# Performance work log

Measured on AMD Instinct MI355X. Metric: run time of the kernel, lower is better.

## Reference

```python
import jax, jax.numpy as jnp
import numpy as np
from jax import lax

B, T, D = 4, 1024, 512      # batch, seq_len, d_model
L = 4                        # n_layers
N = 16                       # d_state
DC = 4                       # d_conv
DI = 2 * D                   # d_inner = expand * d_model
DTR = D // 16                # dt_rank
H = 128                      # head hidden dim
EPS = 1e-5


def layer_norm(x, g, b):
    mu = jnp.mean(x, axis=-1, keepdims=True)
    var = jnp.mean((x - mu) ** 2, axis=-1, keepdims=True)
    return (x - mu) * lax.rsqrt(var + EPS) * g + b


def setup_inputs() -> dict:
    key = jax.random.key(0)
    ks = jax.random.split(key, 24)
    s = 0.02
    return {
        "daily_summaries": jax.random.normal(ks[0], (B, T, D), jnp.float32),
        # per-layer mamba params, stacked on leading L axis
        "in_proj_w": s * jax.random.normal(ks[1], (L, 2 * DI, D), jnp.float32),
        "conv_w": s * jax.random.normal(ks[2], (L, DI, DC), jnp.float32),
        "conv_b": jnp.zeros((L, DI), jnp.float32),
        "x_proj_w": s * jax.random.normal(ks[3], (L, DTR + 2 * N, DI), jnp.float32),
        "dt_proj_w": s * jax.random.normal(ks[4], (L, DI, DTR), jnp.float32),
        "dt_proj_b": jnp.full((L, DI), -4.0, jnp.float32),  # softplus -> small dt
        "A_log": jnp.log(jnp.broadcast_to(jnp.arange(1, N + 1, dtype=jnp.float32), (L, DI, N))),
        "D_skip": jnp.ones((L, DI), jnp.float32),
        "out_proj_w": s * jax.random.normal(ks[5], (L, D, DI), jnp.float32),
        "ln_g": jnp.ones((L, D), jnp.float32),
        "ln_b": jnp.zeros((L, D), jnp.float32),
        # attention pooling
        "attn_w": s * jax.random.normal(ks[6], (1, D), jnp.float32),
        "attn_b": jnp.zeros((1,), jnp.float32),
        # VIX head
        "h1_w": s * jax.random.normal(ks[7], (H, D), jnp.float32),
        "h1_b": jnp.zeros((H,), jnp.float32),
        "ln1_g": jnp.ones((H,), jnp.float32),
        "ln1_b": jnp.zeros((H,), jnp.float32),
        "h2_w": s * jax.random.normal(ks[8], (H, H), jnp.float32),
        "h2_b": jnp.zeros((H,), jnp.float32),
        "ln2_g": jnp.ones((H,), jnp.float32),
        "ln2_b": jnp.zeros((H,), jnp.float32),
        # note: torch zero-inits the final layer; we use random so grads are nonzero
        "h3_w": s * jax.random.normal(ks[9], (1, H), jnp.float32),
        "h3_b": jnp.zeros((1,), jnp.float32),
    }


def mamba_layer(x, in_w, cw, cb, xp_w, dt_w, dt_b, A_log, D_skip, out_w):
    """x: [B,T,D] -> [B,T,D]; canonical Mamba selective scan."""
    xz = jnp.einsum('btd,ed->bte', x, in_w)          # [B,T,2*DI]
    x_in, z = jnp.split(xz, 2, axis=-1)
    # causal depthwise conv over time
    xc = lax.conv_general_dilated(
        x_in.transpose(0, 2, 1), cw[:, None, :], (1,), [(DC - 1, 0)],
        feature_group_count=DI, dimension_numbers=('NCH', 'OIH', 'NCH'))
    xc = jax.nn.silu(xc + cb[None, :, None]).transpose(0, 2, 1)   # [B,T,DI]
    dbc = jnp.einsum('btd,ed->bte', xc, xp_w)        # [B,T,DTR+2N]
    dt_r, Bm, Cm = dbc[..., :DTR], dbc[..., DTR:DTR + N], dbc[..., DTR + N:]
    dt = jax.nn.softplus(jnp.einsum('btr,dr->btd', dt_r, dt_w) + dt_b)  # [B,T,DI]
    A = -jnp.exp(A_log)                              # [DI,N]
    dA = jnp.exp(dt[..., None] * A)                  # [B,T,DI,N]
    dBx = dt[..., None] * Bm[:, :, None, :] * xc[..., None]  # [B,T,DI,N]

    def step(h, inp):
        dA_t, dBx_t, C_t = inp
        h = dA_t * h + dBx_t                         # [B,DI,N]
        return h, jnp.einsum('bdn,bn->bd', h, C_t)

    h0 = jnp.zeros((x.shape[0], DI, N), x.dtype)
    _, ys = lax.scan(step, h0, (dA.transpose(1, 0, 2, 3),
                                dBx.transpose(1, 0, 2, 3),
                                Cm.transpose(1, 0, 2)))
    y = ys.transpose(1, 0, 2) + xc * D_skip          # [B,T,DI]
    y = y * jax.nn.silu(z)
    return jnp.einsum('btd,ed->bte', y, out_w)       # [B,T,D]


def reference(daily_summaries, in_proj_w, conv_w, conv_b, x_proj_w, dt_proj_w,
              dt_proj_b, A_log, D_skip, out_proj_w, ln_g, ln_b, attn_w, attn_b,
              h1_w, h1_b, ln1_g, ln1_b, h2_w, h2_b, ln2_g, ln2_b, h3_w, h3_b):
    x = daily_summaries  # proj is Identity (d_model_l1 == d_model)
    for l in range(L):
        residual = x
        y = mamba_layer(x, in_proj_w[l], conv_w[l], conv_b[l], x_proj_w[l],
                        dt_proj_w[l], dt_proj_b[l], A_log[l], D_skip[l], out_proj_w[l])
        x = layer_norm(y, ln_g[l], ln_b[l]) + residual
    # attention pooling (no mask)
    scores = jnp.einsum('btd,od->bto', x, attn_w) + attn_b   # [B,T,1]
    w = jax.nn.softmax(scores, axis=1)
    pooled = jnp.sum(w * x, axis=1)                          # [B,D]
    # VIX head: Linear -> LN -> GELU (x2) -> Linear
    h1 = jax.nn.gelu(layer_norm(pooled @ h1_w.T + h1_b, ln1_g, ln1_b), approximate=False)
    h2 = jax.nn.gelu(layer_norm(h1 @ h2_w.T + h2_b, ln2_g, ln2_b), approximate=False)
    return (h2 @ h3_w.T + h3_b).squeeze(-1)                  # [B]
```

## Files before the change

kernel.cpp:

```cpp
#include <hip/hip_runtime.h>
#include <hip/hip_bf16.h>
#include <math.h>

#define BATCH 4
#define TLEN 1024
#define DMODEL 512
#define DINNER 1024
#define NSTATE 16
#define EPSV 1e-5f
#define NC 32
#define CT 32
#define DSTR 36
#define LOG2E 1.44269504088896f

typedef __attribute__((ext_vector_type(8))) short bf16x8;
typedef __attribute__((ext_vector_type(4))) float f32x4;

__device__ inline unsigned short f2bf(float f) {
  union { float f; unsigned int u; } c; c.f = f;
  unsigned int u = c.u;
  return (unsigned short)((u + 0x7FFFu + ((u >> 16) & 1u)) >> 16);
}
__device__ inline float bf2f(unsigned short u) {
  union { unsigned int i; float f; } c;
  c.i = ((unsigned int)u) << 16;
  return c.f;
}

__device__ inline float warpReduceSum(float v) {
#pragma unroll
  for (int o = 32; o > 0; o >>= 1) v += __shfl_down(v, o, 64);
  return v;
}
__device__ inline float warpReduceMax(float v) {
#pragma unroll
  for (int o = 32; o > 0; o >>= 1) v = fmaxf(v, __shfl_down(v, o, 64));
  return v;
}
__device__ inline float2 blockReduceSum2_256(float a, float b) {
  __shared__ float sma[4], smb[4];
  int lane = threadIdx.x & 63, wid = threadIdx.x >> 6;
#pragma unroll
  for (int o = 32; o > 0; o >>= 1) { a += __shfl_down(a, o, 64); b += __shfl_down(b, o, 64); }
  if (lane == 0) { sma[wid] = a; smb[wid] = b; }
  __syncthreads();
  float ra = sma[0] + sma[1] + sma[2] + sma[3];
  float rb = smb[0] + smb[1] + smb[2] + smb[3];
  __syncthreads();
  return make_float2(ra, rb);
}
__device__ inline float blockReduceSum256(float v) {
  __shared__ float sm[4];
  int lane = threadIdx.x & 63, wid = threadIdx.x >> 6;
  v = warpReduceSum(v);
  if (lane == 0) sm[wid] = v;
  __syncthreads();
  float r = sm[0] + sm[1] + sm[2] + sm[3];
  __syncthreads();
  return r;
}
__device__ inline float blockReduceMax256(float v) {
  __shared__ float sm[4];
  int lane = threadIdx.x & 63, wid = threadIdx.x >> 6;
  v = warpReduceMax(v);
  if (lane == 0) sm[wid] = v;
  __syncthreads();
  float r = fmaxf(fmaxf(sm[0], sm[1]), fmaxf(sm[2], sm[3]));
  __syncthreads();
  return r;
}
__device__ inline float blockReduceSum128(float v) {
  __shared__ float sm[2];
  int lane = threadIdx.x & 63, wid = threadIdx.x >> 6;
  v = warpReduceSum(v);
  if (lane == 0) sm[wid] = v;
  __syncthreads();
  float r = sm[0] + sm[1];
  __syncthreads();
  return r;
}

__global__ void __launch_bounds__(256)
cast_f32_bf16(const float* __restrict__ src, unsigned short* __restrict__ dst, int n) {
  int i = (blockIdx.x * 256 + threadIdx.x) * 4;
  if (i >= n) return;
  float4 v = *(const float4*)(src + i);
  dst[i + 0] = f2bf(v.x);
  dst[i + 1] = f2bf(v.y);
  dst[i + 2] = f2bf(v.z);
  dst[i + 3] = f2bf(v.w);
}

#define LDP 72
__global__ void __launch_bounds__(256)
gemm_bf16_split(const unsigned short* __restrict__ A, int lda,
                const unsigned short* __restrict__ B, int ldb,
                unsigned short* __restrict__ Cx, unsigned short* __restrict__ Cz, int K) {
  __shared__ unsigned short As[128 * LDP];
  __shared__ unsigned short Bs[128 * LDP];
  const int tid = threadIdx.x;
  const int lane = tid & 63, wid = tid >> 6;
  const int wm = wid >> 1, wn = wid & 1;
  const int row0 = blockIdx.y * 128, col0 = blockIdx.x * 128;
  const int c8 = (tid & 7) * 8;
  const int r0 = tid >> 3;
  const int l15 = lane & 15, lq = lane >> 4;
  f32x4 acc[4][4] = {};
  for (int k0 = 0; k0 < K; k0 += 64) {
#pragma unroll
    for (int p = 0; p < 4; p++) {
      int row = r0 + p * 32;
      bf16x8 av = *(const bf16x8*)(A + (size_t)(row0 + row) * lda + k0 + c8);
      bf16x8 bv = *(const bf16x8*)(B + (size_t)(col0 + row) * ldb + k0 + c8);
      *(bf16x8*)(As + row * LDP + c8) = av;
      *(bf16x8*)(Bs + row * LDP + c8) = bv;
    }
    __syncthreads();
#pragma unroll
    for (int s = 0; s < 2; s++) {
      const int koff = s * 32 + lq * 8;
      bf16x8 af[4], bfr[4];
#pragma unroll
      for (int i = 0; i < 4; i++)
        af[i] = *(const bf16x8*)(As + (wm * 64 + i * 16 + l15) * LDP + koff);
#pragma unroll
      for (int j = 0; j < 4; j++)
        bfr[j] = *(const bf16x8*)(Bs + (wn * 64 + j * 16 + l15) * LDP + koff);
#pragma unroll
      for (int i = 0; i < 4; i++)
#pragma unroll
        for (int j = 0; j < 4; j++)
          acc[i][j] = __builtin_amdgcn_mfma_f32_16x16x32_bf16(af[i], bfr[j], acc[i][j], 0, 0, 0);
    }
    __syncthreads();
  }
  unsigned short* dst = (col0 < 1024) ? Cx : Cz;
  const int cb = (col0 < 1024) ? col0 : (col0 - 1024);
#pragma unroll
  for (int i = 0; i < 4; i++)
#pragma unroll
    for (int j = 0; j < 4; j++)
#pragma unroll
      for (int r = 0; r < 4; r++) {
        int row = row0 + wm * 64 + i * 16 + lq * 4 + r;
        int col = cb + wn * 64 + j * 16 + l15;
        dst[(size_t)row * 1024 + col] = f2bf(acc[i][j][r]);
      }
}

__global__ void __launch_bounds__(256)
gemm_bf16_n64(const unsigned short* __restrict__ A, int lda,
              const unsigned short* __restrict__ B, int ldb,
              float* __restrict__ C, int ldc, int K) {
  __shared__ unsigned short As[128 * LDP];
  __shared__ unsigned short Bs[64 * LDP];
  const int tid = threadIdx.x;
  const int lane = tid & 63, wid = tid >> 6;
  const int wm = wid >> 1, wn = wid & 1;
  const int row0 = blockIdx.y * 128, col0 = blockIdx.x * 64;
  const int c8 = (tid & 7) * 8;
  const int r0 = tid >> 3;
  const int l15 = lane & 15, lq = lane >> 4;
  f32x4 acc[4][2] = {};
  for (int k0 = 0; k0 < K; k0 += 64) {
#pragma unroll
    for (int p = 0; p < 4; p++) {
      int row = r0 + p * 32;
      bf16x8 av = *(const bf16x8*)(A + (size_t)(row0 + row) * lda + k0 + c8);
      *(bf16x8*)(As + row * LDP + c8) = av;
    }
#pragma unroll
    for (int p = 0; p < 2; p++) {
      int row = r0 + p * 32;
      bf16x8 bv = *(const bf16x8*)(B + (size_t)(col0 + row) * ldb + k0 + c8);
      *(bf16x8*)(Bs + row * LDP + c8) = bv;
    }
    __syncthreads();
#pragma unroll
    for (int s = 0; s < 2; s++) {
      const int koff = s * 32 + lq * 8;
      bf16x8 af[4], bfr[2];
#pragma unroll
      for (int i = 0; i < 4; i++)
        af[i] = *(const bf16x8*)(As + (wm * 64 + i * 16 + l15) * LDP + koff);
#pragma unroll
      for (int j = 0; j < 2; j++)
        bfr[j] = *(const bf16x8*)(Bs + (wn * 32 + j * 16 + l15) * LDP + koff);
#pragma unroll
      for (int i = 0; i < 4; i++)
#pragma unroll
        for (int j = 0; j < 2; j++)
          acc[i][j] = __builtin_amdgcn_mfma_f32_16x16x32_bf16(af[i], bfr[j], acc[i][j], 0, 0, 0);
    }
    __syncthreads();
  }
#pragma unroll
  for (int i = 0; i < 4; i++)
#pragma unroll
    for (int j = 0; j < 2; j++)
#pragma unroll
      for (int r = 0; r < 4; r++) {
        int row = row0 + wm * 64 + i * 16 + lq * 4 + r;
        int col = col0 + wn * 32 + j * 16 + l15;
        C[(size_t)row * ldc + col] = acc[i][j][r];
      }
}

__global__ void __launch_bounds__(256)
gemm_bf16_n64_sk(const unsigned short* __restrict__ A, int lda,
                 const unsigned short* __restrict__ B, int ldb,
                 float* __restrict__ Cpart, int KCH) {
  __shared__ unsigned short As[128 * LDP];
  __shared__ unsigned short Bs[64 * LDP];
  const int tid = threadIdx.x;
  const int lane = tid & 63, wid = tid >> 6;
  const int wm = wid >> 1, wn = wid & 1;
  const int row0 = blockIdx.y * 128, col0 = 0;
  const int kbase = blockIdx.z * KCH;
  float* Cz = Cpart + (size_t)blockIdx.z * 4096 * 64;
  const int c8 = (tid & 7) * 8;
  const int r0 = tid >> 3;
  const int l15 = lane & 15, lq = lane >> 4;
  f32x4 acc[4][2] = {};
  for (int k0 = 0; k0 < KCH; k0 += 64) {
#pragma unroll
    for (int p = 0; p < 4; p++) {
      int row = r0 + p * 32;
      bf16x8 av = *(const bf16x8*)(A + (size_t)(row0 + row) * lda + kbase + k0 + c8);
      *(bf16x8*)(As + row * LDP + c8) = av;
    }
#pragma unroll
    for (int p = 0; p < 2; p++) {
      int row = r0 + p * 32;
      bf16x8 bv = *(const bf16x8*)(B + (size_t)(col0 + row) * ldb + kbase + k0 + c8);
      *(bf16x8*)(Bs + row * LDP + c8) = bv;
    }
    __syncthreads();
#pragma unroll
    for (int s = 0; s < 2; s++) {
      const int koff = s * 32 + lq * 8;
      bf16x8 af[4], bfr[2];
#pragma unroll
      for (int i = 0; i < 4; i++)
        af[i] = *(const bf16x8*)(As + (wm * 64 + i * 16 + l15) * LDP + koff);
#pragma unroll
      for (int j = 0; j < 2; j++)
        bfr[j] = *(const bf16x8*)(Bs + (wn * 32 + j * 16 + l15) * LDP + koff);
#pragma unroll
      for (int i = 0; i < 4; i++)
#pragma unroll
        for (int j = 0; j < 2; j++)
          acc[i][j] = __builtin_amdgcn_mfma_f32_16x16x32_bf16(af[i], bfr[j], acc[i][j], 0, 0, 0);
    }
    __syncthreads();
  }
#pragma unroll
  for (int i = 0; i < 4; i++)
#pragma unroll
    for (int j = 0; j < 2; j++)
#pragma unroll
      for (int r = 0; r < 4; r++) {
        int row = row0 + wm * 64 + i * 16 + lq * 4 + r;
        int col = wn * 32 + j * 16 + l15;
        Cz[(size_t)row * 64 + col] = acc[i][j][r];
      }
}

__global__ void __launch_bounds__(256)
reduce4_kernel(const float* __restrict__ part, float* __restrict__ out, int n) {
  int i = (blockIdx.x * 256 + threadIdx.x) * 4;
  if (i >= n) return;
  float4 a = *(const float4*)(part + i);
  float4 b = *(const float4*)(part + n + i);
  float4 c = *(const float4*)(part + 2 * n + i);
  float4 d = *(const float4*)(part + 3 * n + i);
  float4 r;
  r.x = a.x + b.x + c.x + d.x;
  r.y = a.y + b.y + c.y + d.y;
  r.z = a.z + b.z + c.z + d.z;
  r.w = a.w + b.w + c.w + d.w;
  *(float4*)(out + i) = r;
}

__global__ void __launch_bounds__(256)
gemm_dt(const float* __restrict__ A, const float* __restrict__ B,
        unsigned short* __restrict__ C, const float* __restrict__ bias) {
  __shared__ __align__(16) float As[16][68];
  __shared__ __align__(16) float Bs[16][68];
  const int tid = threadIdx.x;
  const int tx = tid & 15, ty = tid >> 4;
  const int row0 = blockIdx.y * 64, col0 = blockIdx.x * 64;
  float acc[4][4] = {};
  for (int k0 = 0; k0 < 32; k0 += 16) {
#pragma unroll
    for (int i = 0; i < 4; i++) {
      int e = tid + i * 256;
      int m = e >> 4, kk = e & 15;
      As[kk][m] = A[(size_t)(row0 + m) * 64 + k0 + kk];
      Bs[kk][m] = B[(size_t)(col0 + m) * 32 + k0 + kk];
    }
    __syncthreads();
#pragma unroll
    for (int kk = 0; kk < 16; kk++) {
      float4 a4 = *(const float4*)&As[kk][ty << 2];
      float4 b4 = *(const float4*)&Bs[kk][tx << 2];
      float a[4] = {a4.x, a4.y, a4.z, a4.w};
      float b[4] = {b4.x, b4.y, b4.z, b4.w};
#pragma unroll
      for (int i = 0; i < 4; i++)
#pragma unroll
        for (int j = 0; j < 4; j++) acc[i][j] = fmaf(a[i], b[j], acc[i][j]);
    }
    __syncthreads();
  }
#pragma unroll
  for (int i = 0; i < 4; i++) {
    size_t r = row0 + (ty << 2) + i;
#pragma unroll
    for (int j = 0; j < 4; j++) {
      int c = col0 + (tx << 2) + j;
      float v = acc[i][j] + bias[c];
      v = (v > 20.f) ? v : log1pf(__expf(v));
      C[r * 1024 + c] = f2bf(v);
    }
  }
}

__global__ void conv_silu_kernel(const unsigned short* __restrict__ xinbf,
                                 const float* __restrict__ cw,
                                 const float* __restrict__ cb,
                                 unsigned short* __restrict__ xcbf) {
  int idx = blockIdx.x * 256 + threadIdx.x;
  int d = idx & 1023;
  int bt = idx >> 10;
  int t = bt & 1023;
  float acc = cb[d];
  const float* w = cw + d * 4;
#pragma unroll
  for (int k = 0; k < 4; k++) {
    int ts = t - 3 + k;
    if (ts >= 0) acc = fmaf(bf2f(xinbf[((size_t)bt + (ts - t)) * 1024 + d]), w[k], acc);
  }
  float sig = 1.f / (1.f + __expf(-acc));
  xcbf[idx] = f2bf(acc * sig);
}

__global__ void __launch_bounds__(256)
scan_part1(const unsigned short* __restrict__ dtbf, const unsigned short* __restrict__ xcbf,
           const float* __restrict__ dbc, const float* __restrict__ A_log,
           float* __restrict__ hloc, float* __restrict__ sdtb) {
  __shared__ unsigned short dts[64 * DSTR];
  __shared__ unsigned short xcs[64 * DSTR];
  __shared__ float Bsh[CT * 20];
  const int chunk = blockIdx.x, dg = blockIdx.y, b = blockIdx.z;
  const int tid = threadIdx.x;
  const int ch = tid >> 2, q4 = (tid & 3) * 4;
  const int d = dg * 64 + ch;
  const size_t bt0 = (size_t)b * TLEN + chunk * CT;
  for (int i = tid; i < CT * 64; i += 256) {
    int t = i >> 6, c = i & 63;
    size_t bt = bt0 + t;
    dts[c * DSTR + t] = dtbf[bt * 1024 + dg * 64 + c];
    xcs[c * DSTR + t] = xcbf[bt * 1024 + dg * 64 + c];
  }
  for (int i = tid; i < CT * 16; i += 256) {
    int t = i >> 4, n = i & 15;
    Bsh[t * 20 + n] = dbc[(bt0 + t) * 64 + 32 + n];
  }
  __syncthreads();
  float4 al = *(const float4*)&A_log[d * 16 + q4];
  float4 A;
  A.x = -__expf(al.x) * LOG2E; A.y = -__expf(al.y) * LOG2E;
  A.z = -__expf(al.z) * LOG2E; A.w = -__expf(al.w) * LOG2E;
  float4 h = {0.f, 0.f, 0.f, 0.f};
  float sdt = 0.f;
#pragma unroll
  for (int t0 = 0; t0 < CT; t0 += 4) {
    ushort4 d4 = *(const ushort4*)&dts[ch * DSTR + t0];
    ushort4 x4 = *(const ushort4*)&xcs[ch * DSTR + t0];
    const float dta[4] = {bf2f(d4.x), bf2f(d4.y), bf2f(d4.z), bf2f(d4.w)};
    const float xca[4] = {bf2f(x4.x), bf2f(x4.y), bf2f(x4.z), bf2f(x4.w)};
#pragma unroll
    for (int u = 0; u < 4; u++) {
      float dtv = dta[u];
      float4 B4 = *(const float4*)&Bsh[(t0 + u) * 20 + q4];
      float uin = dtv * xca[u];
      h.x = fmaf(exp2f(dtv * A.x), h.x, uin * B4.x);
      h.y = fmaf(exp2f(dtv * A.y), h.y, uin * B4.y);
      h.z = fmaf(exp2f(dtv * A.z), h.z, uin * B4.z);
      h.w = fmaf(exp2f(dtv * A.w), h.w, uin * B4.w);
      sdt += dtv;
    }
  }
  size_t slab = (size_t)(b * 16 + dg);
  *(float4*)&hloc[(slab * NC + chunk) * 1024 + tid * 4] = h;
  sdtb[(slab * NC + chunk) * 256 + tid] = sdt;
}

__global__ void __launch_bounds__(256)
scan_prefix(const float* __restrict__ A_log, const float* __restrict__ hloc,
            const float* __restrict__ sdtb, float* __restrict__ h0buf) {
  const int slab = blockIdx.x;
  const int tid = threadIdx.x;
  const int dg = slab & 15;
  const int ch = tid >> 2, q4 = (tid & 3) * 4;
  const int d = dg * 64 + ch;
  float4 al = *(const float4*)&A_log[d * 16 + q4];
  float4 A;
  A.x = -__expf(al.x) * LOG2E; A.y = -__expf(al.y) * LOG2E;
  A.z = -__expf(al.z) * LOG2E; A.w = -__expf(al.w) * LOG2E;
  float4 h = {0.f, 0.f, 0.f, 0.f};
  size_t base = (size_t)slab * NC;
  for (int c = 0; c < NC; c++) {
    *(float4*)&h0buf[(base + c) * 1024 + tid * 4] = h;
    float4 hl = *(const float4*)&hloc[(base + c) * 1024 + tid * 4];
    float s = sdtb[(base + c) * 256 + tid];
    h.x = fmaf(exp2f(s * A.x), h.x, hl.x);
    h.y = fmaf(exp2f(s * A.y), h.y, hl.y);
    h.z = fmaf(exp2f(s * A.z), h.z, hl.z);
    h.w = fmaf(exp2f(s * A.w), h.w, hl.w);
  }
}

__global__ void __launch_bounds__(256)
scan_part2(const unsigned short* __restrict__ dtbf, const unsigned short* __restrict__ xcbf,
           const float* __restrict__ dbc, const unsigned short* __restrict__ zbf,
           const float* __restrict__ A_log, const float* __restrict__ Dsk,
           const float* __restrict__ h0buf, unsigned short* __restrict__ ybf) {
  __shared__ unsigned short dts[64 * DSTR];
  __shared__ unsigned short xcs[64 * DSTR];
  __shared__ float Bsh[CT * 20];
  __shared__ float Csh[CT * 20];
  __shared__ float ys[CT * 64];
  const int chunk = blockIdx.x, dg = blockIdx.y, b = blockIdx.z;
  const int tid = threadIdx.x;
  const int q = tid & 3;
  const int ch = tid >> 2, q4 = q * 4;
  const int d = dg * 64 + ch;
  const size_t bt0 = (size_t)b * TLEN + chunk * CT;
  const size_t slab = (size_t)(b * 16 + dg);
  float4 h = *(const float4*)&h0buf[(slab * NC + chunk) * 1024 + tid * 4];
  float4 al = *(const float4*)&A_log[d * 16 + q4];
  float4 A;
  A.x = -__expf(al.x) * LOG2E; A.y = -__expf(al.y) * LOG2E;
  A.z = -__expf(al.z) * LOG2E; A.w = -__expf(al.w) * LOG2E;
  for (int i = tid; i < CT * 64; i += 256) {
    int t = i >> 6, c = i & 63;
    size_t bt = bt0 + t;
    dts[c * DSTR + t] = dtbf[bt * 1024 + dg * 64 + c];
    xcs[c * DSTR + t] = xcbf[bt * 1024 + dg * 64 + c];
  }
  for (int i = tid; i < CT * 16; i += 256) {
    int t = i >> 4, n = i & 15;
    Bsh[t * 20 + n] = dbc[(bt0 + t) * 64 + 32 + n];
    Csh[t * 20 + n] = dbc[(bt0 + t) * 64 + 48 + n];
  }
  __syncthreads();
  const float Dv = Dsk[d];
#pragma unroll
  for (int t0 = 0; t0 < CT; t0 += 4) {
    ushort4 d4 = *(const ushort4*)&dts[ch * DSTR + t0];
    ushort4 x4 = *(const ushort4*)&xcs[ch * DSTR + t0];
    const float dta[4] = {bf2f(d4.x), bf2f(d4.y), bf2f(d4.z), bf2f(d4.w)};
    const float xca[4] = {bf2f(x4.x), bf2f(x4.y), bf2f(x4.z), bf2f(x4.w)};
#pragma unroll
    for (int u = 0; u < 4; u++) {
      float dtv = dta[u];
      float4 B4 = *(const float4*)&Bsh[(t0 + u) * 20 + q4];
      float4 C4 = *(const float4*)&Csh[(t0 + u) * 20 + q4];
      float uin = dtv * xca[u];
      h.x = fmaf(exp2f(dtv * A.x), h.x, uin * B4.x);
      h.y = fmaf(exp2f(dtv * A.y), h.y, uin * B4.y);
      h.z = fmaf(exp2f(dtv * A.z), h.z, uin * B4.z);
      h.w = fmaf(exp2f(dtv * A.w), h.w, uin * B4.w);
      float cs = h.x * C4.x + h.y * C4.y + h.z * C4.z + h.w * C4.w;
      cs += __shfl_xor(cs, 1, 4);
      cs += __shfl_xor(cs, 2, 4);
      if (q == 0) ys[(t0 + u) * 64 + ch] = cs + xca[u] * Dv;
    }
  }
  __syncthreads();
  for (int i = tid; i < CT * 64; i += 256) {
    int t = i >> 6, c = i & 63;
    size_t bt = bt0 + t;
    float zv = bf2f(zbf[bt * 1024 + dg * 64 + c]);
    float sig = 1.f / (1.f + __expf(-zv));
    ybf[bt * 1024 + dg * 64 + c] = f2bf(ys[t * 64 + c] * (zv * sig));
  }
}

__global__ void __launch_bounds__(256)
ln_res_kernel(const float* __restrict__ mo, const float* __restrict__ res,
              const float* __restrict__ g, const float* __restrict__ bb,
              float* __restrict__ xout, unsigned short* __restrict__ xout_bf) {
  int row = blockIdx.x;
  int tid = threadIdx.x;
  size_t base = (size_t)row * 512;
  float v0 = mo[base + tid], v1 = mo[base + tid + 256];
  float2 ss = blockReduceSum2_256(v0 + v1, v0 * v0 + v1 * v1);
  float mu = ss.x * (1.f / 512.f);
  float var = ss.y * (1.f / 512.f) - mu * mu;
  float rs = rsqrtf(var + EPSV);
  float o0 = (v0 - mu) * rs * g[tid] + bb[tid] + res[base + tid];
  float o1 = (v1 - mu) * rs * g[tid + 256] + bb[tid + 256] + res[base + tid + 256];
  xout[base + tid] = o0;
  xout[base + tid + 256] = o1;
  xout_bf[base + tid] = f2bf(o0);
  xout_bf[base + tid + 256] = f2bf(o1);
}

__global__ void __launch_bounds__(256)
score_kernel(const unsigned short* __restrict__ x, const float* __restrict__ aw,
             const float* __restrict__ ab, float* __restrict__ sc) {
  int row = blockIdx.x * 4 + (threadIdx.x >> 6);
  int lane = threadIdx.x & 63;
  size_t base = (size_t)row * 512;
  float p = 0.f;
#pragma unroll
  for (int j = 0; j < 8; j++)
    p = fmaf(bf2f(x[base + lane + 64 * j]), aw[lane + 64 * j], p);
  p = warpReduceSum(p);
  if (lane == 0) sc[row] = p + ab[0];
}

__global__ void __launch_bounds__(256)
softmax_t_kernel(const float* __restrict__ sc, float* __restrict__ wsm) {
  int b = blockIdx.x, tid = threadIdx.x;
  float v[4];
  float m = -INFINITY;
#pragma unroll
  for (int j = 0; j < 4; j++) { v[j] = sc[b * 1024 + tid + 256 * j]; m = fmaxf(m, v[j]); }
  m = blockReduceMax256(m);
  float s = 0.f;
#pragma unroll
  for (int j = 0; j < 4; j++) { v[j] = __expf(v[j] - m); s += v[j]; }
  s = blockReduceSum256(s);
  float inv = 1.f / s;
#pragma unroll
  for (int j = 0; j < 4; j++) wsm[b * 1024 + tid + 256 * j] = v[j] * inv;
}

__global__ void __launch_bounds__(256)
pool_partial(const unsigned short* __restrict__ x, const float* __restrict__ wsm,
             float* __restrict__ partial) {
  int tc = blockIdx.x, b = blockIdx.y, tid = threadIdx.x;
  float a0 = 0.f, a1 = 0.f;
  for (int t = tc * 32; t < tc * 32 + 32; t++) {
    float wv = wsm[b * 1024 + t];
    size_t base = ((size_t)b * 1024 + t) * 512;
    a0 = fmaf(wv, bf2f(x[base + tid]), a0);
    a1 = fmaf(wv, bf2f(x[base + tid + 256]), a1);
  }
  size_t pb = ((size_t)b * 32 + tc) * 512;
  partial[pb + tid] = a0;
  partial[pb + tid + 256] = a1;
}

__global__ void __launch_bounds__(256)
pool_reduce(const float* __restrict__ partial, float* __restrict__ pooled) {
  int b = blockIdx.x, tid = threadIdx.x;
  float a0 = 0.f, a1 = 0.f;
  for (int tc = 0; tc < 32; tc++) {
    size_t pb = ((size_t)b * 32 + tc) * 512;
    a0 += partial[pb + tid];
    a1 += partial[pb + tid + 256];
  }
  pooled[b * 512 + tid] = a0;
  pooled[b * 512 + tid + 256] = a1;
}

__device__ inline float gelu_exact(float x) {
  return 0.5f * x * (1.f + erff(x * 0.70710678118654752f));
}
__global__ void __launch_bounds__(128)
head_kernel(const float* __restrict__ pooled,
            const float* __restrict__ h1w, const float* __restrict__ h1b,
            const float* __restrict__ g1, const float* __restrict__ b1,
            const float* __restrict__ h2w, const float* __restrict__ h2b,
            const float* __restrict__ g2, const float* __restrict__ b2,
            const float* __restrict__ h3w, const float* __restrict__ h3b,
            float* __restrict__ out) {
  int tid = threadIdx.x;
  int b = blockIdx.x;
  __shared__ float hs[128];
  float s = h1b[tid];
  const float* p = pooled + b * 512;
  for (int d = 0; d < 512; d += 4) {
    float4 pv = *(const float4*)(p + d);
    float4 wv = *(const float4*)(h1w + tid * 512 + d);
    s = fmaf(pv.x, wv.x, s); s = fmaf(pv.y, wv.y, s);
    s = fmaf(pv.z, wv.z, s); s = fmaf(pv.w, wv.w, s);
  }
  float mu = blockReduceSum128(s) * (1.f / 128.f);
  float dd = s - mu;
  float var = blockReduceSum128(dd * dd) * (1.f / 128.f);
  float v = dd * rsqrtf(var + EPSV) * g1[tid] + b1[tid];
  hs[tid] = gelu_exact(v);
  __syncthreads();
  float s2 = h2b[tid];
  for (int j = 0; j < 128; j++) s2 = fmaf(hs[j], h2w[tid * 128 + j], s2);
  float mu2 = blockReduceSum128(s2) * (1.f / 128.f);
  float d2 = s2 - mu2;
  float var2 = blockReduceSum128(d2 * d2) * (1.f / 128.f);
  float v2 = d2 * rsqrtf(var2 + EPSV) * g2[tid] + b2[tid];
  float h2v = gelu_exact(v2);
  float o = blockReduceSum128(h2v * h3w[tid]);
  if (tid == 0) out[b] = o + h3b[0];
}

extern "C" void kernel_launch(void* const* d_in, const int* in_sizes, int n_in,
                              void* d_out, int out_size, void* d_ws, size_t ws_size,
                              hipStream_t stream) {
  (void)in_sizes; (void)n_in; (void)out_size; (void)ws_size;
  const float* x0   = (const float*)d_in[0];
  const float* inw  = (const float*)d_in[1];
  const float* cw   = (const float*)d_in[2];
  const float* cb   = (const float*)d_in[3];
  const float* xpw  = (const float*)d_in[4];
  const float* dtw  = (const float*)d_in[5];
  const float* dtb  = (const float*)d_in[6];
  const float* alog = (const float*)d_in[7];
  const float* dsk  = (const float*)d_in[8];
  const float* outw = (const float*)d_in[9];
  const float* lng  = (const float*)d_in[10];
  const float* lnb  = (const float*)d_in[11];
  const float* aw   = (const float*)d_in[12];
  const float* ab   = (const float*)d_in[13];
  const float* h1w  = (const float*)d_in[14];
  const float* h1b  = (const float*)d_in[15];
  const float* g1   = (const float*)d_in[16];
  const float* b1   = (const float*)d_in[17];
  const float* h2w  = (const float*)d_in[18];
  const float* h2b  = (const float*)d_in[19];
  const float* g2   = (const float*)d_in[20];
  const float* b2   = (const float*)d_in[21];
  const float* h3w  = (const float*)d_in[22];
  const float* h3b  = (const float*)d_in[23];

  float* ws = (float*)d_ws;
  unsigned short* xinbf = (unsigned short*)ws;
  unsigned short* zbf   = xinbf + 4194304;
  unsigned short* xcbf  = zbf + 4194304;
  unsigned short* dtbf  = xcbf + 4194304;
  float* dbc     = (float*)(dtbf + 4194304);
  float* xpart   = dbc + 262144;
  float* mo      = xpart + 1048576;
  float* xbuf    = mo + 2097152;
  float* hloc    = xbuf + 2097152;
  float* sdtb    = hloc + 2097152;
  float* h0buf   = sdtb + 524288;
  float* scores  = h0buf + 2097152;
  float* wsm     = scores + 4096;
  float* partial = wsm + 4096;
  float* pooled  = partial + 65536;
  unsigned short* abuf    = (unsigned short*)(pooled + 2048);
  unsigned short* ybf     = abuf + 2097152;
  unsigned short* wbf_in  = ybf + 4194304;
  unsigned short* wbf_out = wbf_in + 4194304;
  unsigned short* wbf_xp  = wbf_out + 2097152;

  cast_f32_bf16<<<4096, 256, 0, stream>>>(inw, wbf_in, 4194304);
  cast_f32_bf16<<<2048, 256, 0, stream>>>(outw, wbf_out, 2097152);
  cast_f32_bf16<<<256, 256, 0, stream>>>(xpw, wbf_xp, 262144);
  cast_f32_bf16<<<2048, 256, 0, stream>>>(x0, abuf, 2097152);

  const float* xcur = x0;
  for (int l = 0; l < 4; l++) {
    gemm_bf16_split<<<dim3(16, 32), 256, 0, stream>>>(
        abuf, 512, wbf_in + (size_t)l * 2048 * 512, 512, xinbf, zbf, 512);
    conv_silu_kernel<<<16384, 256, 0, stream>>>(xinbf, cw + l * 4096, cb + l * 1024, xcbf);
    gemm_bf16_n64_sk<<<dim3(1, 32, 4), 256, 0, stream>>>(
        xcbf, 1024, wbf_xp + (size_t)l * 65536, 1024, xpart, 256);
    reduce4_kernel<<<256, 256, 0, stream>>>(xpart, dbc, 262144);
    gemm_dt<<<dim3(16, 64), 256, 0, stream>>>(
        dbc, dtw + (size_t)l * 32768, dtbf, dtb + l * 1024);
    scan_part1<<<dim3(NC, 16, 4), 256, 0, stream>>>(
        dtbf, xcbf, dbc, alog + (size_t)l * 16384, hloc, sdtb);
    scan_prefix<<<64, 256, 0, stream>>>(alog + (size_t)l * 16384, hloc, sdtb, h0buf);
    scan_part2<<<dim3(NC, 16, 4), 256, 0, stream>>>(
        dtbf, xcbf, dbc, zbf, alog + (size_t)l * 16384, dsk + l * 1024, h0buf, ybf);
    gemm_bf16_n64<<<dim3(8, 32), 256, 0, stream>>>(
        ybf, 1024, wbf_out + (size_t)l * 524288, 1024, mo, 512, 1024);
    ln_res_kernel<<<4096, 256, 0, stream>>>(mo, xcur, lng + l * 512, lnb + l * 512,
                                            xbuf, abuf);
    xcur = xbuf;
  }
  score_kernel<<<1024, 256, 0, stream>>>(abuf, aw, ab, scores);
  softmax_t_kernel<<<4, 256, 0, stream>>>(scores, wsm);
  pool_partial<<<dim3(32, 4), 256, 0, stream>>>(abuf, wsm, partial);
  pool_reduce<<<4, 256, 0, stream>>>(partial, pooled);
  head_kernel<<<4, 128, 0, stream>>>(pooled, h1w, h1b, g1, b1, h2w, h2b, g2, b2,
                                     h3w, h3b, (float*)d_out);
}
```

Before: 762.2 us.

## Fuse dt projection into scan kernels, vectorize conv, fold scores into layernorm

Removes the separate gemm_dt kernel and its bf16 dt buffer. Each scan kernel now computes dt = softplus(dbc[:, :32] @ dt_w^T + b) in shared memory from the dbc tile it already loads. The depthwise conv+SiLU kernel now processes four channels per thread with vector loads. The attention score dot product is folded into the final layer's layernorm kernel, which drops score_kernel. The trade-off is that the dt projection is computed twice, once in each scan pass, and shared memory use per block goes up.

Result: slower. 778.7 us (+2.2%).

```diff
diff --git a/kernel.cpp b/kernel.cpp
--- a/kernel.cpp
+++ b/kernel.cpp
@@ -215,7 +215,7 @@
   const int tid = threadIdx.x;
   const int lane = tid & 63, wid = tid >> 6;
   const int wm = wid >> 1, wn = wid & 1;
-  const int row0 = blockIdx.y * 128, col0 = 0;
+  const int row0 = blockIdx.y * 128;
   const int kbase = blockIdx.z * KCH;
   float* Cz = Cpart + (size_t)blockIdx.z * 4096 * 64;
   const int c8 = (tid & 7) * 8;
@@ -232,7 +232,7 @@
 #pragma unroll
     for (int p = 0; p < 2; p++) {
       int row = r0 + p * 32;
-      bf16x8 bv = *(const bf16x8*)(B + (size_t)(col0 + row) * ldb + kbase + k0 + c8);
+      bf16x8 bv = *(const bf16x8*)(B + (size_t)row * ldb + kbase + k0 + c8);
       *(bf16x8*)(Bs + row * LDP + c8) = bv;
     }
     __syncthreads();
@@ -283,75 +283,52 @@
 }
 
 __global__ void __launch_bounds__(256)
-gemm_dt(const float* __restrict__ A, const float* __restrict__ B,
-        unsigned short* __restrict__ C, const float* __restrict__ bias) {
-  __shared__ __align__(16) float As[16][68];
-  __shared__ __align__(16) float Bs[16][68];
-  const int tid = threadIdx.x;
-  const int tx = tid & 15, ty = tid >> 4;
-  const int row0 = blockIdx.y * 64, col0 = blockIdx.x * 64;
-  float acc[4][4] = {};
-  for (int k0 = 0; k0 < 32; k0 += 16) {
-#pragma unroll
-    for (int i = 0; i < 4; i++) {
-      int e = tid + i * 256;
-      int m = e >> 4, kk = e & 15;
-      As[kk][m] = A[(size_t)(row0 + m) * 64 + k0 + kk];
-      Bs[kk][m] = B[(size_t)(col0 + m) * 32 + k0 + kk];
-    }
-    __syncthreads();
-#pragma unroll
-    for (int kk = 0; kk < 16; kk++) {
-      float4 a4 = *(const float4*)&As[kk][ty << 2];
-      float4 b4 = *(const float4*)&Bs[kk][tx << 2];
-      float a[4] = {a4.x, a4.y, a4.z, a4.w};
-      float b[4] = {b4.x, b4.y, b4.z, b4.w};
-#pragma unroll
-      for (int i = 0; i < 4; i++)
-#pragma unroll
-        for (int j = 0; j < 4; j++) acc[i][j] = fmaf(a[i], b[j], acc[i][j]);
-    }
-    __syncthreads();
-  }
-#pragma unroll
-  for (int i = 0; i < 4; i++) {
-    size_t r = row0 + (ty << 2) + i;
-#pragma unroll
-    for (int j = 0; j < 4; j++) {
-      int c = col0 + (tx << 2) + j;
-      float v = acc[i][j] + bias[c];
-      v = (v > 20.f) ? v : log1pf(__expf(v));
-      C[r * 1024 + c] = f2bf(v);
-    }
-  }
-}
-
-__global__ void conv_silu_kernel(const unsigned short* __restrict__ xinbf,
-                                 const float* __restrict__ cw,
-                                 const float* __restrict__ cb,
-                                 unsigned short* __restrict__ xcbf) {
+conv_silu_kernel(const unsigned short* __restrict__ xinbf,
+                 const float* __restrict__ cw,
+                 const float* __restrict__ cb,
+                 unsigned short* __restrict__ xcbf) {
   int idx = blockIdx.x * 256 + threadIdx.x;
-  int d = idx & 1023;
-  int bt = idx >> 10;
+  int d4 = (idx & 255) * 4;
+  int bt = idx >> 8;
   int t = bt & 1023;
-  float acc = cb[d];
-  const float* w = cw + d * 4;
+  float4 bias4 = *(const float4*)(cb + d4);
+  float a0 = bias4.x, a1 = bias4.y, a2 = bias4.z, a3 = bias4.w;
+  float4 w0 = *(const float4*)(cw + (size_t)(d4 + 0) * 4);
+  float4 w1 = *(const float4*)(cw + (size_t)(d4 + 1) * 4);
+  float4 w2 = *(const float4*)(cw + (size_t)(d4 + 2) * 4);
+  float4 w3 = *(const float4*)(cw + (size_t)(d4 + 3) * 4);
+  const float k0[4] = {w0.x, w0.y, w0.z, w0.w};
+  const float k1[4] = {w1.x, w1.y, w1.z, w1.w};
+  const float k2[4] = {w2.x, w2.y, w2.z, w2.w};
+  const float k3[4] = {w3.x, w3.y, w3.z, w3.w};
 #pragma unroll
   for (int k = 0; k < 4; k++) {
     int ts = t - 3 + k;
-    if (ts >= 0) acc = fmaf(bf2f(xinbf[((size_t)bt + (ts - t)) * 1024 + d]), w[k], acc);
-  }
-  float sig = 1.f / (1.f + __expf(-acc));
-  xcbf[idx] = f2bf(acc * sig);
-}
-
-__global__ void __launch_bounds__(256)
-scan_part1(const unsigned short* __restrict__ dtbf, const unsigned short* __restrict__ xcbf,
-           const float* __restrict__ dbc, const float* __restrict__ A_log,
+    if (ts >= 0) {
+      ushort4 xv = *(const ushort4*)(xinbf + ((size_t)bt + (ts - t)) * 1024 + d4);
+      a0 = fmaf(bf2f(xv.x), k0[k], a0);
+      a1 = fmaf(bf2f(xv.y), k1[k], a1);
+      a2 = fmaf(bf2f(xv.z), k2[k], a2);
+      a3 = fmaf(bf2f(xv.w), k3[k], a3);
+    }
+  }
+  ushort4 outv;
+  outv.x = f2bf(a0 / (1.f + __expf(-a0)));
+  outv.y = f2bf(a1 / (1.f + __expf(-a1)));
+  outv.z = f2bf(a2 / (1.f + __expf(-a2)));
+  outv.w = f2bf(a3 / (1.f + __expf(-a3)));
+  *(ushort4*)(xcbf + (size_t)bt * 1024 + d4) = outv;
+}
+
+__global__ void __launch_bounds__(256)
+scan_part1(const unsigned short* __restrict__ xcbf,
+           const float* __restrict__ dbc, const float* __restrict__ dtw,
+           const float* __restrict__ dtbias, const float* __restrict__ A_log,
            float* __restrict__ hloc, float* __restrict__ sdtb) {
+  __shared__ float dbcs[CT * 68];
+  __shared__ float dtws[64 * 33];
   __shared__ unsigned short dts[64 * DSTR];
   __shared__ unsigned short xcs[64 * DSTR];
-  __shared__ float Bsh[CT * 20];
   const int chunk = blockIdx.x, dg = blockIdx.y, b = blockIdx.z;
   const int tid = threadIdx.x;
   const int ch = tid >> 2, q4 = (tid & 3) * 4;
@@ -359,13 +336,27 @@
   const size_t bt0 = (size_t)b * TLEN + chunk * CT;
   for (int i = tid; i < CT * 64; i += 256) {
     int t = i >> 6, c = i & 63;
-    size_t bt = bt0 + t;
-    dts[c * DSTR + t] = dtbf[bt * 1024 + dg * 64 + c];
-    xcs[c * DSTR + t] = xcbf[bt * 1024 + dg * 64 + c];
-  }
-  for (int i = tid; i < CT * 16; i += 256) {
-    int t = i >> 4, n = i & 15;
-    Bsh[t * 20 + n] = dbc[(bt0 + t) * 64 + 32 + n];
+    dbcs[t * 68 + c] = dbc[(bt0 + t) * 64 + c];
+    xcs[c * DSTR + t] = xcbf[(bt0 + t) * 1024 + dg * 64 + c];
+  }
+  for (int i = tid; i < 64 * 32; i += 256) {
+    int c = i >> 5, k = i & 31;
+    dtws[c * 33 + k] = dtw[(size_t)(dg * 64 + c) * 32 + k];
+  }
+  __syncthreads();
+  {
+    const int chd = tid & 63, tq = tid >> 6;
+    const float bias = dtbias[dg * 64 + chd];
+#pragma unroll
+    for (int jj = 0; jj < 8; jj++) {
+      int t = tq * 8 + jj;
+      float acc = bias;
+#pragma unroll
+      for (int k = 0; k < 32; k++)
+        acc = fmaf(dbcs[t * 68 + k], dtws[chd * 33 + k], acc);
+      acc = (acc > 20.f) ? acc : log1pf(__expf(acc));
+      dts[chd * DSTR + t] = f2bf(acc);
+    }
   }
   __syncthreads();
   float4 al = *(const float4*)&A_log[d * 16 + q4];
@@ -383,7 +374,7 @@
 #pragma unroll
     for (int u = 0; u < 4; u++) {
       float dtv = dta[u];
-      float4 B4 = *(const float4*)&Bsh[(t0 + u) * 20 + q4];
+      float4 B4 = *(const float4*)&dbcs[(t0 + u) * 68 + 32 + q4];
       float uin = dtv * xca[u];
       h.x = fmaf(exp2f(dtv * A.x), h.x, uin * B4.x);
       h.y = fmaf(exp2f(dtv * A.y), h.y, uin * B4.y);
@@ -423,15 +414,15 @@
 }
 
 __global__ void __launch_bounds__(256)
-scan_part2(const unsigned short* __restrict__ dtbf, const unsigned short* __restrict__ xcbf,
-           const float* __restrict__ dbc, const unsigned short* __restrict__ zbf,
+scan_part2(const unsigned short* __restrict__ xcbf,
+           const float* __restrict__ dbc, const float* __restrict__ dtw,
+           const float* __restrict__ dtbias, const unsigned short* __restrict__ zbf,
            const float* __restrict__ A_log, const float* __restrict__ Dsk,
            const float* __restrict__ h0buf, unsigned short* __restrict__ ybf) {
+  __shared__ float dbcs[CT * 68];
+  __shared__ float poolbuf[64 * 33];
   __shared__ unsigned short dts[64 * DSTR];
   __shared__ unsigned short xcs[64 * DSTR];
-  __shared__ float Bsh[CT * 20];
-  __shared__ float Csh[CT * 20];
-  __shared__ float ys[CT * 64];
   const int chunk = blockIdx.x, dg = blockIdx.y, b = blockIdx.z;
   const int tid = threadIdx.x;
   const int q = tid & 3;
@@ -446,16 +437,30 @@
   A.z = -__expf(al.z) * LOG2E; A.w = -__expf(al.w) * LOG2E;
   for (int i = tid; i < CT * 64; i += 256) {
     int t = i >> 6, c = i & 63;
-    size_t bt = bt0 + t;
-    dts[c * DSTR + t] = dtbf[bt * 1024 + dg * 64 + c];
-    xcs[c * DSTR + t] = xcbf[bt * 1024 + dg * 64 + c];
-  }
-  for (int i = tid; i < CT * 16; i += 256) {
-    int t = i >> 4, n = i & 15;
-    Bsh[t * 20 + n] = dbc[(bt0 + t) * 64 + 32 + n];
-    Csh[t * 20 + n] = dbc[(bt0 + t) * 64 + 48 + n];
-  }
-  __syncthreads();
+    dbcs[t * 68 + c] = dbc[(bt0 + t) * 64 + c];
+    xcs[c * DSTR + t] = xcbf[(bt0 + t) * 1024 + dg * 64 + c];
+  }
+  for (int i = tid; i < 64 * 32; i += 256) {
+    int c = i >> 5, k = i & 31;
+    poolbuf[c * 33 + k] = dtw[(size_t)(dg * 64 + c) * 32 + k];
+  }
+  __syncthreads();
+  {
+    const int chd = tid & 63, tq = tid >> 6;
+    const float bias = dtbias[dg * 64 + chd];
+#pragma unroll
+    for (int jj = 0; jj < 8; jj++) {
+      int t = tq * 8 + jj;
+      float acc = bias;
+#pragma unroll
+      for (int k = 0; k < 32; k++)
+        acc = fmaf(dbcs[t * 68 + k], poolbuf[chd * 33 + k], acc);
+      acc = (acc > 20.f) ? acc : log1pf(__expf(acc));
+      dts[chd * DSTR + t] = f2bf(acc);
+    }
+  }
+  __syncthreads();
+  float* ys = poolbuf;
   const float Dv = Dsk[d];
 #pragma unroll
   for (int t0 = 0; t0 < CT; t0 += 4) {
@@ -466,8 +471,8 @@
 #pragma unroll
     for (int u = 0; u < 4; u++) {
       float dtv = dta[u];
-      float4 B4 = *(const float4*)&Bsh[(t0 + u) * 20 + q4];
-      float4 C4 = *(const float4*)&Csh[(t0 + u) * 20 + q4];
+      float4 B4 = *(const float4*)&dbcs[(t0 + u) * 68 + 32 + q4];
+      float4 C4 = *(const float4*)&dbcs[(t0 + u) * 68 + 48 + q4];
       float uin = dtv * xca[u];
       h.x = fmaf(exp2f(dtv * A.x), h.x, uin * B4.x);
       h.y = fmaf(exp2f(dtv * A.y), h.y, uin * B4.y);
@@ -492,7 +497,9 @@
 __global__ void __launch_bounds__(256)
 ln_res_kernel(const float* __restrict__ mo, const float* __restrict__ res,
               const float* __restrict__ g, const float* __restrict__ bb,
-              float* __restrict__ xout, unsigned short* __restrict__ xout_bf) {
+              float* __restrict__ xout, unsigned short* __restrict__ xout_bf,
+              const float* __restrict__ awv, const float* __restrict__ abv,
+              float* __restrict__ scores) {
   int row = blockIdx.x;
   int tid = threadIdx.x;
   size_t base = (size_t)row * 512;
@@ -507,20 +514,11 @@
   xout[base + tid + 256] = o1;
   xout_bf[base + tid] = f2bf(o0);
   xout_bf[base + tid + 256] = f2bf(o1);
-}
-
-__global__ void __launch_bounds__(256)
-score_kernel(const unsigned short* __restrict__ x, const float* __restrict__ aw,
-             const float* __restrict__ ab, float* __restrict__ sc) {
-  int row = blockIdx.x * 4 + (threadIdx.x >> 6);
-  int lane = threadIdx.x & 63;
-  size_t base = (size_t)row * 512;
-  float p = 0.f;
-#pragma unroll
-  for (int j = 0; j < 8; j++)
-    p = fmaf(bf2f(x[base + lane + 64 * j]), aw[lane + 64 * j], p);
-  p = warpReduceSum(p);
-  if (lane == 0) sc[row] = p + ab[0];
+  if (awv != nullptr) {
+    float sp = o0 * awv[tid] + o1 * awv[tid + 256];
+    float s = blockReduceSum256(sp);
+    if (tid == 0) scores[row] = s + abv[0];
+  }
 }
 
 __global__ void __launch_bounds__(256)
@@ -641,8 +639,7 @@
   unsigned short* xinbf = (unsigned short*)ws;
   unsigned short* zbf   = xinbf + 4194304;
   unsigned short* xcbf  = zbf + 4194304;
-  unsigned short* dtbf  = xcbf + 4194304;
-  float* dbc     = (float*)(dtbf + 4194304);
+  float* dbc     = (float*)(xcbf + 4194304);
   float* xpart   = dbc + 262144;
   float* mo      = xpart + 1048576;
   float* xbuf    = mo + 2097152;
@@ -668,24 +665,24 @@
   for (int l = 0; l < 4; l++) {
     gemm_bf16_split<<<dim3(16, 32), 256, 0, stream>>>(
         abuf, 512, wbf_in + (size_t)l * 2048 * 512, 512, xinbf, zbf, 512);
-    conv_silu_kernel<<<16384, 256, 0, stream>>>(xinbf, cw + l * 4096, cb + l * 1024, xcbf);
+    conv_silu_kernel<<<4096, 256, 0, stream>>>(xinbf, cw + l * 4096, cb + l * 1024, xcbf);
     gemm_bf16_n64_sk<<<dim3(1, 32, 4), 256, 0, stream>>>(
         xcbf, 1024, wbf_xp + (size_t)l * 65536, 1024, xpart, 256);
     reduce4_kernel<<<256, 256, 0, stream>>>(xpart, dbc, 262144);
-    gemm_dt<<<dim3(16, 64), 256, 0, stream>>>(
-        dbc, dtw + (size_t)l * 32768, dtbf, dtb + l * 1024);
     scan_part1<<<dim3(NC, 16, 4), 256, 0, stream>>>(
-        dtbf, xcbf, dbc, alog + (size_t)l * 16384, hloc, sdtb);
+        xcbf, dbc, dtw + (size_t)l * 32768, dtb + l * 1024,
+        alog + (size_t)l * 16384, hloc, sdtb);
     scan_prefix<<<64, 256, 0, stream>>>(alog + (size_t)l * 16384, hloc, sdtb, h0buf);
     scan_part2<<<dim3(NC, 16, 4), 256, 0, stream>>>(
-        dtbf, xcbf, dbc, zbf, alog + (size_t)l * 16384, dsk + l * 1024, h0buf, ybf);
+        xcbf, dbc, dtw + (size_t)l * 32768, dtb + l * 1024, zbf,
+        alog + (size_t)l * 16384, dsk + l * 1024, h0buf, ybf);
     gemm_bf16_n64<<<dim3(8, 32), 256, 0, stream>>>(
         ybf, 1024, wbf_out + (size_t)l * 524288, 1024, mo, 512, 1024);
-    ln_res_kernel<<<4096, 256, 0, stream>>>(mo, xcur, lng + l * 512, lnb + l * 512,
-                                            xbuf, abuf);
+    ln_res_kernel<<<4096, 256, 0, stream>>>(
+        mo, xcur, lng + l * 512, lnb + l * 512, xbuf, abuf,
+        (l == 3) ? aw : nullptr, ab, scores);
     xcur = xbuf;
   }
-  score_kernel<<<1024, 256, 0, stream>>>(abuf, aw, ab, scores);
   softmax_t_kernel<<<4, 256, 0, stream>>>(scores, wsm);
   pool_partial<<<dim3(32, 4), 256, 0, stream>>>(abuf, wsm, partial);
   pool_reduce<<<4, 256, 0, stream>>>(partial, pooled);
```
